# Kernel optimization log

Measured on AMD Instinct MI355X. Metric: run time of the kernel, lower is better.

## Reference

```python
import jax, jax.numpy as jnp
import numpy as np

TINY = 1e-6
SGNUM = 12

def _ln(x, g, b):
    m = jnp.mean(x, -1, keepdims=True)
    v = jnp.mean((x - m) ** 2, -1, keepdims=True)
    return (x - m) * jax.lax.rsqrt(v + 1e-5) * g + b

def _mean_var(x, w):
    # weighted mean/variance over the view dim (-2), keepdim
    mean = jnp.sum(x * w, -2, keepdims=True)
    var = jnp.sum(w * (x - mean) ** 2, -2, keepdims=True)
    return mean, var

def setup_inputs():
    BN, H, W, N = 1, 128, 128, 8
    CTX, PF, PH, HD, MH, FH = 61, 32, 64, 32, 256, 128
    D = CTX + 3 + PF  # 96
    key = jax.random.key(0)
    ks = iter(jax.random.split(key, 64))
    def rnm(shape):
        return jax.random.normal(next(ks), shape, jnp.float32)
    def pw(shape):
        return jax.random.normal(next(ks), shape, jnp.float32) * 0.02
    inp = dict(
        rgb=jax.random.uniform(next(ks), (BN, H, W, N, 3), jnp.float32),
        featmaps_dense=rnm((BN, H, W, 1, CTX)),
        view_dir=rnm((BN, H, W, N, 3)),
        proj_err=rnm((BN, H, W, N, 1)),
        normal=rnm((BN, H, W, 1, 3)),
        DL=rnm((BN, H, W, SGNUM * 7)),
        # pbr_mlp: LN(7) -> Lin(7,PH) ELU -> Lin(PH,PH) ELU -> Lin(PH,PH) ELU -> Lin(PH,PF)
        pbr_ln_g=jnp.ones((7,), jnp.float32), pbr_ln_b=jnp.zeros((7,), jnp.float32),
        pbr_w1=pw((7, PH)), pbr_b1=jnp.zeros((PH,), jnp.float32),
        pbr_w2=pw((PH, PH)), pbr_b2=jnp.zeros((PH,), jnp.float32),
        pbr_w3=pw((PH, PH)), pbr_b3=jnp.zeros((PH,), jnp.float32),
        pbr_w4=pw((PH, PF)), pbr_b4=jnp.zeros((PF,), jnp.float32),
        # transformer block 1
        tv1_ln_g=jnp.ones((D,), jnp.float32), tv1_ln_b=jnp.zeros((D,), jnp.float32),
        tv1_w=pw((D, HD)),
        to1_w=pw((3 * HD, D)), to1_b=jnp.zeros((D,), jnp.float32),
        n1_ln_g=jnp.ones((D,), jnp.float32), n1_ln_b=jnp.zeros((D,), jnp.float32),
        n1_w1=pw((D, MH)), n1_b1=jnp.zeros((MH,), jnp.float32),
        n1_w2=pw((MH, D)), n1_b2=jnp.zeros((D,), jnp.float32),
        # transformer block 2
        tv2_ln_g=jnp.ones((D,), jnp.float32), tv2_ln_b=jnp.zeros((D,), jnp.float32),
        tv2_w=pw((D, HD)),
        to2_w=pw((3 * HD, D)), to2_b=jnp.zeros((D,), jnp.float32),
        n2_ln_g=jnp.ones((D,), jnp.float32), n2_ln_b=jnp.zeros((D,), jnp.float32),
        n2_w1=pw((D, MH)), n2_b1=jnp.zeros((MH,), jnp.float32),
        n2_w2=pw((MH, D)), n2_b2=jnp.zeros((D,), jnp.float32),
        # mlp_brdf
        brdf_ln_g=jnp.ones((D,), jnp.float32), brdf_ln_b=jnp.zeros((D,), jnp.float32),
        brdf_w1=pw((D, FH)), brdf_b1=jnp.zeros((FH,), jnp.float32),
        brdf_w2=pw((FH, FH)), brdf_b2=jnp.zeros((FH,), jnp.float32),
    )
    return inp

def reference(rgb, featmaps_dense, view_dir, proj_err, normal, DL,
              pbr_ln_g, pbr_ln_b, pbr_w1, pbr_b1, pbr_w2, pbr_b2, pbr_w3, pbr_b3, pbr_w4, pbr_b4,
              tv1_ln_g, tv1_ln_b, tv1_w, to1_w, to1_b,
              n1_ln_g, n1_ln_b, n1_w1, n1_b1, n1_w2, n1_b2,
              tv2_ln_g, tv2_ln_b, tv2_w, to2_w, to2_b,
              n2_ln_g, n2_ln_b, n2_w1, n2_b1, n2_w2, n2_b2,
              brdf_ln_g, brdf_ln_b, brdf_w1, brdf_b1, brdf_w2, brdf_b2):
    bn, h, w, n, _ = rgb.shape
    # view weights from reprojection error
    wgt = -jnp.minimum(jnp.log10(jnp.abs(proj_err) + TINY), 0.0)
    wgt = wgt / (jnp.sum(wgt, -2, keepdims=True) + TINY)  # [bn,h,w,n,1]
    DL6 = DL.reshape(bn, h, w, 1, SGNUM, 7)
    dl_dir = DL6[..., :3]
    DLdotN = jnp.sum(dl_dir * normal[:, :, :, :, None, :], -1, keepdims=True)  # [bn,h,w,1,SG,1]
    hdotV = (jnp.sum(dl_dir * view_dir[:, :, :, :, None, :], -1, keepdims=True) + 1.0) * 0.5  # [bn,h,w,n,SG,1]
    fresnel = jnp.exp2((-5.55472 * hdotV - 6.98316) * hdotV)
    VdotN = jnp.sum(view_dir * normal, -1, keepdims=True)[..., None, :]  # [bn,h,w,n,1,1]
    part = jnp.broadcast_to(jnp.concatenate([DLdotN, DL6[..., 3:]], -1), (bn, h, w, n, SGNUM, 5))
    VdotN = jnp.broadcast_to(VdotN, (bn, h, w, n, SGNUM, 1))
    pbr = jnp.concatenate([part, fresnel, VdotN], -1)  # [bn,h,w,n,SG,7]
    y = _ln(pbr, pbr_ln_g, pbr_ln_b)
    y = jax.nn.elu(y @ pbr_w1 + pbr_b1)
    y = jax.nn.elu(y @ pbr_w2 + pbr_b2)
    y = jax.nn.elu(y @ pbr_w3 + pbr_b3)
    pbr_feature = jnp.sum(y @ pbr_w4 + pbr_b4, -2)  # sum over SGNum -> [bn,h,w,n,PF]
    fm = jnp.broadcast_to(featmaps_dense, (bn, h, w, n, featmaps_dense.shape[-1]))
    x_input = jnp.concatenate([rgb, fm, pbr_feature], -1)  # [bn,h,w,n,D]
    # transformer block 1
    v = _ln(x_input, tv1_ln_g, tv1_ln_b) @ tv1_w  # [bn,h,w,n,HD]
    mean, var = _mean_var(v, wgt)
    mv = jnp.broadcast_to(jnp.concatenate([mean, var], -1), v.shape[:-1] + (2 * v.shape[-1],))
    x = jnp.concatenate([v, mv], -1) @ to1_w + to1_b + x_input
    x = jax.nn.gelu(_ln(x, n1_ln_g, n1_ln_b) @ n1_w1 + n1_b1, approximate=False) @ n1_w2 + n1_b2 + x_input
    # transformer block 2 (collapses view dim)
    v = _ln(x, tv2_ln_g, tv2_ln_b) @ tv2_w
    mean, var = _mean_var(v, wgt)
    x = (jnp.concatenate([v[..., :1, :], mean, var], -1) @ to2_w + to2_b)[..., 0, :]
    x = x + x_input[..., 0, :]
    x = jax.nn.gelu(_ln(x, n2_ln_g, n2_ln_b) @ n2_w1 + n2_b1, approximate=False) @ n2_w2 + n2_b2 + x_input[..., 0, :]
    brdf = jax.nn.gelu(_ln(x, brdf_ln_g, brdf_ln_b) @ brdf_w1 + brdf_b1, approximate=False) @ brdf_w2 + brdf_b2
    return brdf  # [bn,h,w,final_hidden]
```

## Files before the change

kernel.cpp:

```cpp
#include <hip/hip_runtime.h>
#include <math.h>


#define NPIX 16384

__device__ __forceinline__ float elu_f(float x){ return x > 0.f ? x : (__expf(x) - 1.f); }
__device__ __forceinline__ float gelu_f(float x){ return 0.5f*x*(1.f + erff(x*0.70710678118654752f)); }

__device__ __forceinline__ void fma4(float4& a, float s, const float4 w){
  a.x = fmaf(s, w.x, a.x); a.y = fmaf(s, w.y, a.y);
  a.z = fmaf(s, w.z, a.z); a.w = fmaf(s, w.w, a.w);
}
__device__ __forceinline__ float4 elu4f(float4 a){
  return make_float4(elu_f(a.x), elu_f(a.y), elu_f(a.z), elu_f(a.w));
}

#define NTA 768
#define NBA (NPIX/2)

constexpr int AYA   = 0;
constexpr int AYB   = 13056;
constexpr int AWB   = 26112;
constexpr int AXL   = 30208;
constexpr int ABIAS = 31744;
constexpr int ATOT  = 31968;

template<int K, int SI, bool DOELU>
__device__ __forceinline__ void mmA64(const float* __restrict__ Xin,
                                      const float* __restrict__ WB,
                                      const float* __restrict__ bias,
                                      float* __restrict__ Yout, int t)
{
  const int rq = t >> 4, c4 = t & 15;
  const float* x0 = Xin + (4*rq+0)*SI;
  const float* x1 = Xin + (4*rq+1)*SI;
  const float* x2 = Xin + (4*rq+2)*SI;
  const float* x3 = Xin + (4*rq+3)*SI;
  const float4* __restrict__ W4 = (const float4*)WB;
  const float4 b = ((const float4*)bias)[c4];
  float4 a0=b, a1=b, a2=b, a3=b;
  #pragma unroll
  for (int k2 = 0; k2 < K/2; ++k2){
    const float2 xa = *(const float2*)(x0 + 2*k2);
    const float2 xb = *(const float2*)(x1 + 2*k2);
    const float2 xc = *(const float2*)(x2 + 2*k2);
    const float2 xd = *(const float2*)(x3 + 2*k2);
    const float4 wA = W4[(2*k2)*16 + c4];
    const float4 wB = W4[(2*k2+1)*16 + c4];
    fma4(a0, xa.x, wA); fma4(a0, xa.y, wB);
    fma4(a1, xb.x, wA); fma4(a1, xb.y, wB);
    fma4(a2, xc.x, wA); fma4(a2, xc.y, wB);
    fma4(a3, xd.x, wA); fma4(a3, xd.y, wB);
  }
  if (DOELU){ a0 = elu4f(a0); a1 = elu4f(a1); a2 = elu4f(a2); a3 = elu4f(a3); }
  *(float4*)(Yout + (4*rq+0)*68 + 4*c4) = a0;
  *(float4*)(Yout + (4*rq+1)*68 + 4*c4) = a1;
  *(float4*)(Yout + (4*rq+2)*68 + 4*c4) = a2;
  *(float4*)(Yout + (4*rq+3)*68 + 4*c4) = a3;
}

__device__ __forceinline__ void mmA32(const float* __restrict__ Xin,
                                      const float* __restrict__ WB,
                                      const float* __restrict__ bias,
                                      float* __restrict__ F, int t)
{
  const int rq = t >> 4, c2 = t & 15;
  const float* x0 = Xin + (4*rq+0)*68;
  const float* x1 = Xin + (4*rq+1)*68;
  const float* x2 = Xin + (4*rq+2)*68;
  const float* x3 = Xin + (4*rq+3)*68;
  const float2* __restrict__ W2 = (const float2*)WB;
  const float2 b = ((const float2*)bias)[c2];
  float2 a0=b, a1=b, a2=b, a3=b;
  #pragma unroll
  for (int k2 = 0; k2 < 32; ++k2){
    const float2 xa = *(const float2*)(x0 + 2*k2);
    const float2 xb = *(const float2*)(x1 + 2*k2);
    const float2 xc = *(const float2*)(x2 + 2*k2);
    const float2 xd = *(const float2*)(x3 + 2*k2);
    const float2 wA = W2[(2*k2)*16 + c2];
    const float2 wB = W2[(2*k2+1)*16 + c2];
    a0.x = fmaf(xa.x, wA.x, a0.x); a0.y = fmaf(xa.x, wA.y, a0.y);
    a0.x = fmaf(xa.y, wB.x, a0.x); a0.y = fmaf(xa.y, wB.y, a0.y);
    a1.x = fmaf(xb.x, wA.x, a1.x); a1.y = fmaf(xb.x, wA.y, a1.y);
    a1.x = fmaf(xb.y, wB.x, a1.x); a1.y = fmaf(xb.y, wB.y, a1.y);
    a2.x = fmaf(xc.x, wA.x, a2.x); a2.y = fmaf(xc.x, wA.y, a2.y);
    a2.x = fmaf(xc.y, wB.x, a2.x); a2.y = fmaf(xc.y, wB.y, a2.y);
    a3.x = fmaf(xd.x, wA.x, a3.x); a3.y = fmaf(xd.x, wA.y, a3.y);
    a3.x = fmaf(xd.y, wB.x, a3.x); a3.y = fmaf(xd.y, wB.y, a3.y);
  }
  *(float2*)(F + (4*rq+0)*34 + 2*c2) = a0;
  *(float2*)(F + (4*rq+1)*34 + 2*c2) = a1;
  *(float2*)(F + (4*rq+2)*34 + 2*c2) = a2;
  *(float2*)(F + (4*rq+3)*34 + 2*c2) = a3;
}

__global__ __launch_bounds__(NTA)
void mva_phaseA(const float* __restrict__ view_dir, const float* __restrict__ normal,
                const float* __restrict__ DL,
                const float* __restrict__ ln_g, const float* __restrict__ ln_b,
                const float* __restrict__ w1, const float* __restrict__ b1,
                const float* __restrict__ w2, const float* __restrict__ b2,
                const float* __restrict__ w3, const float* __restrict__ b3,
                const float* __restrict__ w4, const float* __restrict__ b4,
                float* __restrict__ feat)
{
  __shared__ __align__(16) float smem[ATOT];
  const int t = threadIdx.x;
  const int bpx0 = blockIdx.x*2;
  float4* WB4 = (float4*)(smem + AWB);

  {
    const float4* s = (const float4*)w1;
    for (int i = t; i < 128; i += NTA){
      const int k = i >> 4, c4 = i & 15;
      WB4[i] = (k < 7) ? s[k*16 + c4] : make_float4(0.f,0.f,0.f,0.f);
    }
    float4* d = (float4*)(smem+ABIAS);
    if (t >= 256 && t < 272)      d[t-256]      = ((const float4*)b1)[t-256];
    else if (t >= 272 && t < 288) d[16 + t-272] = ((const float4*)b2)[t-272];
    else if (t >= 288 && t < 304) d[32 + t-288] = ((const float4*)b3)[t-288];
    else if (t >= 304 && t < 312) d[48 + t-304] = ((const float4*)b4)[t-304];
  }
  if (t < 192){
    const int pl = t / 96, rr = t - pl*96;
    const int sg = rr >> 3, view = rr & 7;
    const int px = bpx0 + pl;
    const float nm0 = normal[px*3+0], nm1 = normal[px*3+1], nm2 = normal[px*3+2];
    const float* vd = view_dir + (px*8 + view)*3;
    const float vd0 = vd[0], vd1 = vd[1], vd2 = vd[2];
    const float* dl = DL + px*84 + sg*7;
    const float d0=dl[0], d1=dl[1], d2=dl[2], d3=dl[3], d4=dl[4], d5=dl[5], d6=dl[6];

    const float DLdotN = d0*nm0 + d1*nm1 + d2*nm2;
    const float hv     = (d0*vd0 + d1*vd1 + d2*vd2 + 1.f)*0.5f;
    const float fres   = exp2f((-5.55472f*hv - 6.98316f)*hv);
    const float VdotN  = vd0*nm0 + vd1*nm1 + vd2*nm2;

    const float x0 = DLdotN, x1 = d3, x2 = d4, x3 = d5, x4 = d6, x5 = fres, x6 = VdotN;
    const float m  = (x0+x1+x2+x3+x4+x5+x6)*(1.f/7.f);
    float q, var = 0.f;
    q = x0-m; var += q*q; q = x1-m; var += q*q; q = x2-m; var += q*q;
    q = x3-m; var += q*q; q = x4-m; var += q*q; q = x5-m; var += q*q;
    q = x6-m; var += q*q;
    const float rs = rsqrtf(var*(1.f/7.f) + 1e-5f);
    float* xl = smem + AXL + t*8;
    xl[0] = (x0-m)*rs*ln_g[0] + ln_b[0];
    xl[1] = (x1-m)*rs*ln_g[1] + ln_b[1];
    xl[2] = (x2-m)*rs*ln_g[2] + ln_b[2];
    xl[3] = (x3-m)*rs*ln_g[3] + ln_b[3];
    xl[4] = (x4-m)*rs*ln_g[4] + ln_b[4];
    xl[5] = (x5-m)*rs*ln_g[5] + ln_b[5];
    xl[6] = (x6-m)*rs*ln_g[6] + ln_b[6];
    xl[7] = 0.f;
  }
  __syncthreads();

  float4 p0 = ((const float4*)w2)[t];
  float4 p1 = (t < 256) ? ((const float4*)w2)[t + 768] : make_float4(0.f,0.f,0.f,0.f);
  mmA64<8,8,true>(smem+AXL, smem+AWB, smem+ABIAS+0, smem+AYA, t);
  __syncthreads();
  WB4[t] = p0; if (t < 256) WB4[t + 768] = p1;
  __syncthreads();

  p0 = ((const float4*)w3)[t];
  p1 = (t < 256) ? ((const float4*)w3)[t + 768] : make_float4(0.f,0.f,0.f,0.f);
  mmA64<64,68,true>(smem+AYA, smem+AWB, smem+ABIAS+64, smem+AYB, t);
  __syncthreads();
  WB4[t] = p0; if (t < 256) WB4[t + 768] = p1;
  __syncthreads();

  p0 = (t < 512) ? ((const float4*)w4)[t] : make_float4(0.f,0.f,0.f,0.f);
  mmA64<64,68,true>(smem+AYB, smem+AWB, smem+ABIAS+128, smem+AYA, t);
  __syncthreads();
  if (t < 512) WB4[t] = p0;
  __syncthreads();

  mmA32(smem+AYA, smem+AWB, smem+ABIAS+192, smem+AYB, t);
  __syncthreads();

  if (t < 512){
    const int pl = t >> 8, idx = t & 255;
    const int v = idx >> 5, c = idx & 31;
    float s = 0.f;
    #pragma unroll
    for (int sg = 0; sg < 12; ++sg) s += smem[AYB + (pl*96 + sg*8 + v)*34 + c];
    feat[(size_t)(bpx0 + pl)*256 + idx] = s;
  }
}

#define NTB 512

template<int KK, int CC, int LDWG>
__device__ __forceinline__ void stageW(const float* __restrict__ Wg, int c4off,
                                       float* __restrict__ wbuf, int t)
{
  constexpr int C4 = CC/4;
  constexpr int N4 = KK*C4;
  const float4* __restrict__ s = (const float4*)Wg;
  float4* d = (float4*)wbuf;
  for (int i = t; i < N4; i += NTB){
    const int k = i / C4, c4 = i - k*C4;
    d[i] = s[k*(LDWG/4) + c4off + c4];
  }
}

__device__ __forceinline__ void ln32s(const float* __restrict__ in, int Si,
                                      float* __restrict__ out, int So,
                                      const float* __restrict__ g, const float* __restrict__ b,
                                      int t)
{
  if (t < 256){
    const int r = t >> 3, l8 = t & 7;
    const float* row = in + r*Si;
    float vals[12]; int cols[12];
    float s1 = 0.f, s2 = 0.f;
    #pragma unroll
    for (int i = 0; i < 12; ++i){
      int c = l8 + 8*i + 8*(r & 7); if (c >= 96) c -= 96;
      float a = row[c];
      cols[i] = c; vals[i] = a; s1 += a; s2 += a*a;
    }
    s1 += __shfl_xor(s1, 1); s2 += __shfl_xor(s2, 1);
    s1 += __shfl_xor(s1, 2); s2 += __shfl_xor(s2, 2);
    s1 += __shfl_xor(s1, 4); s2 += __shfl_xor(s2, 4);
    float mean = s1*(1.f/96.f);
    float var  = s2*(1.f/96.f) - mean*mean;
    float rsd = rsqrtf(var + 1e-5f);
    float* orow = out + r*So;
    #pragma unroll
    for (int i = 0; i < 12; ++i){
      int c = cols[i];
      orow[c] = (vals[i]-mean)*rsd*g[c] + b[c];
    }
  }
}

template<int K, int C, int LDW, bool GELU, bool HASB, bool RES, bool ACC>
__device__ __forceinline__ void mmR32(const float* __restrict__ inb, int S,
                                      const float* __restrict__ Wl, const float* __restrict__ bg,
                                      float* __restrict__ outb, int So,
                                      const float* __restrict__ residb, int Sr, int t)
{
  constexpr int C4 = C/4;
  const float4* __restrict__ W4 = (const float4*)Wl;
  for (int gi = t; gi < C4*16; gi += NTB){
    const int rp = gi & 15, c4 = gi >> 4;
    const float2* x0 = (const float2*)(inb + (2*rp)*S);
    const float2* x1 = (const float2*)(inb + (2*rp+1)*S);
    float4 a0 = HASB ? ((const float4*)bg)[c4] : make_float4(0.f,0.f,0.f,0.f);
    float4 a1 = a0;
    #pragma unroll 8
    for (int k2 = 0; k2 < K/2; ++k2){
      float2 xa = x0[k2], xb = x1[k2];
      float4 wA = W4[(2*k2)*(LDW/4) + c4];
      float4 wB = W4[(2*k2+1)*(LDW/4) + c4];
      fma4(a0, xa.x, wA); fma4(a0, xa.y, wB);
      fma4(a1, xb.x, wA); fma4(a1, xb.y, wB);
    }
    if (GELU){
      a0.x=gelu_f(a0.x); a0.y=gelu_f(a0.y); a0.z=gelu_f(a0.z); a0.w=gelu_f(a0.w);
      a1.x=gelu_f(a1.x); a1.y=gelu_f(a1.y); a1.z=gelu_f(a1.z); a1.w=gelu_f(a1.w);
    }
    if (RES){
      const float* r0 = residb + (2*rp)*Sr + 4*c4;
      const float* r1 = residb + (2*rp+1)*Sr + 4*c4;
      a0.x += r0[0]; a0.y += r0[1]; a0.z += r0[2]; a0.w += r0[3];
      a1.x += r1[0]; a1.y += r1[1]; a1.z += r1[2]; a1.w += r1[3];
    }
    float* o0 = outb + (2*rp)*So + 4*c4;
    float* o1 = outb + (2*rp+1)*So + 4*c4;
    if (ACC){
      a0.x += o0[0]; a0.y += o0[1]; a0.z += o0[2]; a0.w += o0[3];
      a1.x += o1[0]; a1.y += o1[1]; a1.z += o1[2]; a1.w += o1[3];
    }
    o0[0]=a0.x; o0[1]=a0.y; o0[2]=a0.z; o0[3]=a0.w;
    o1[0]=a1.x; o1[1]=a1.y; o1[2]=a1.z; o1[3]=a1.w;
  }
}

#define NBB1 (NPIX/4)
constexpr int BXIN  = 0;
constexpr int BXCUR = 3264;
constexpr int BXLN  = 6528;
constexpr int BHID  = 9792;
constexpr int BVB   = 14080;
constexpr int BMEAN = 15296;
constexpr int BVAR  = 15424;
constexpr int BWGT  = 15552;
constexpr int BWBUF = 15584;
constexpr int B1TOT = 27872;

__global__ __launch_bounds__(NTB)
void mva_phaseB1(const float* __restrict__ rgb, const float* __restrict__ fm,
                 const float* __restrict__ proj_err, float* __restrict__ ws,
                 const float* __restrict__ tv1_ln_g, const float* __restrict__ tv1_ln_b,
                 const float* __restrict__ tv1_w,
                 const float* __restrict__ to1_w, const float* __restrict__ to1_b,
                 const float* __restrict__ n1_ln_g, const float* __restrict__ n1_ln_b,
                 const float* __restrict__ n1_w1, const float* __restrict__ n1_b1,
                 const float* __restrict__ n1_w2, const float* __restrict__ n1_b2,
                 const float* __restrict__ tv2_ln_g, const float* __restrict__ tv2_ln_b,
                 const float* __restrict__ tv2_w)
{
  __shared__ __align__(16) float smem[B1TOT];
  const int t = threadIdx.x;
  const int bpx0 = blockIdx.x*4;
  float* WB = smem + BWBUF;

  for (int u = t; u < 2048; u += NTB){
    const int r = u >> 6, k = u & 63;
    const int pl = r >> 3, v = r & 7;
    float val = (k < 3) ? rgb[((bpx0+pl)*8 + v)*3 + k]
                        : fm[(bpx0+pl)*61 + (k-3)];
    smem[BXIN + r*102 + k] = val;
  }
  for (int u = t; u < 1024; u += NTB){
    const int r = u >> 5, c = u & 31;
    smem[BXIN + r*102 + 64 + c] = ws[(size_t)blockIdx.x*1024 + u];
  }
  if (t < 32){
    float pe = proj_err[(bpx0 + (t>>3))*8 + (t&7)];
    float wraw = fmaxf(-log10f(fabsf(pe) + 1e-6f), 0.f);
    float s = wraw;
    s += __shfl_xor(s, 1); s += __shfl_xor(s, 2); s += __shfl_xor(s, 4);
    smem[BWGT + t] = wraw / (s + 1e-6f);
  }
  stageW<96,32,32>(tv1_w, 0, WB, t);
  __syncthreads();

  ln32s(smem+BXIN, 102, smem+BXLN, 102, tv1_ln_g, tv1_ln_b, t);
  __syncthreads();
  mmR32<96,32,32,false,false,false,false>(smem+BXLN, 102, WB, nullptr, smem+BVB, 38, nullptr, 0, t);
  __syncthreads();
  if (t < 128){
    const int pl = t >> 5, c = t & 31;
    const float* wn = smem + BWGT + pl*8;
    float m = 0.f;
    #pragma unroll
    for (int v = 0; v < 8; ++v) m += wn[v]*smem[BVB + (pl*8+v)*38 + c];
    float vv = 0.f;
    #pragma unroll
    for (int v = 0; v < 8; ++v){ float d = smem[BVB + (pl*8+v)*38 + c] - m; vv += wn[v]*d*d; }
    smem[BMEAN + pl*32 + c] = m;
    smem[BVAR  + pl*32 + c] = vv;
  }
  __syncthreads();
  for (int u = t; u < 3072; u += NTB){
    const int r = u & 31, c = u >> 5;
    const int pl = r >> 3;
    float val = (c < 32) ? smem[BVB + r*38 + c]
              : (c < 64) ? smem[BMEAN + pl*32 + (c-32)]
                         : smem[BVAR + pl*32 + (c-64)];
    smem[BXLN + r*102 + c] = val;
  }
  stageW<96,96,96>(to1_w, 0, WB, t);
  __syncthreads();
  mmR32<96,96,96,false,true,true,false>(smem+BXLN, 102, WB, to1_b, smem+BXCUR, 102, smem+BXIN, 102, t);
  __syncthreads();

  ln32s(smem+BXCUR, 102, smem+BXLN, 102, n1_ln_g, n1_ln_b, t);
  __syncthreads();
  stageW<96,128,256>(n1_w1, 0, WB, t);
  __syncthreads();
  mmR32<96,128,128,true,true,false,false>(smem+BXLN, 102, WB, n1_b1, smem+BHID, 134, nullptr, 0, t);
  __syncthreads();
  stageW<128,96,96>(n1_w2, 0, WB, t);
  __syncthreads();
  mmR32<128,96,96,false,false,false,false>(smem+BHID, 134, WB, nullptr, smem+BXCUR, 102, nullptr, 0, t);
  __syncthreads();
  stageW<96,128,256>(n1_w1, 32, WB, t);
  __syncthreads();
  mmR32<96,128,128,true,true,false,false>(smem+BXLN, 102, WB, n1_b1 + 128, smem+BHID, 134, nullptr, 0, t);
  __syncthreads();
  stageW<128,96,96>(n1_w2 + 128*96, 0, WB, t);
  __syncthreads();
  mmR32<128,96,96,false,true,true,true>(smem+BHID, 134, WB, n1_b2, smem+BXCUR, 102, smem+BXIN, 102, t);
  __syncthreads();

  ln32s(smem+BXCUR, 102, smem+BXLN, 102, tv2_ln_g, tv2_ln_b, t);
  stageW<96,32,32>(tv2_w, 0, WB, t);
  __syncthreads();
  mmR32<96,32,32,false,false,false,false>(smem+BXLN, 102, WB, nullptr, smem+BVB, 38, nullptr, 0, t);
  __syncthreads();
  if (t < 128){
    const int pl = t >> 5, c = t & 31;
    const float* wn = smem + BWGT + pl*8;
    float m = 0.f;
    #pragma unroll
    for (int v = 0; v < 8; ++v) m += wn[v]*smem[BVB + (pl*8+v)*38 + c];
    float vv = 0.f;
    #pragma unroll
    for (int v = 0; v < 8; ++v){ float d = smem[BVB + (pl*8+v)*38 + c] - m; vv += wn[v]*d*d; }
    smem[BMEAN + pl*32 + c] = m;
    smem[BVAR  + pl*32 + c] = vv;
  }
  __syncthreads();
  if (t < 384){
    const int pl = t / 96, c = t - pl*96;
    float val = (c < 32) ? smem[BVB + (pl*8)*38 + c]
              : (c < 64) ? smem[BMEAN + pl*32 + (c-32)]
                         : smem[BVAR + pl*32 + (c-64)];
    ws[(size_t)blockIdx.x*1024 + pl*256 + 96 + c] = val;
  }
}

#define NBB2 (NPIX/32)
constexpr int CXLN  = 0;
constexpr int CXIN  = 3264;
constexpr int CXS   = 6528;
constexpr int CTMP  = 9792;
constexpr int CHID  = 13056;
constexpr int CWBUF = 17344;
constexpr int B2TOT = 29632;

__global__ __launch_bounds__(NTB)
void mva_phaseB2(const float* __restrict__ rgb, const float* __restrict__ fm,
                 const float* __restrict__ ws,
                 const float* __restrict__ to2_w, const float* __restrict__ to2_b,
                 const float* __restrict__ n2_ln_g, const float* __restrict__ n2_ln_b,
                 const float* __restrict__ n2_w1, const float* __restrict__ n2_b1,
                 const float* __restrict__ n2_w2, const float* __restrict__ n2_b2,
                 const float* __restrict__ brdf_ln_g, const float* __restrict__ brdf_ln_b,
                 const float* __restrict__ brdf_w1, const float* __restrict__ brdf_b1,
                 const float* __restrict__ brdf_w2, const float* __restrict__ brdf_b2,
                 float* __restrict__ out)
{
  __shared__ __align__(16) float smem[B2TOT];
  const int t = threadIdx.x;
  const int bpx0 = blockIdx.x*32;
  float* WB = smem + CWBUF;

  for (int u = t; u < 3072; u += NTB){
    const int r = u / 96, c = u - r*96;
    const int px = bpx0 + r;
    const size_t ab = (size_t)px*256;
    smem[CXLN + r*102 + c] = ws[ab + 96 + c];
    float xv = (c < 3)  ? rgb[((size_t)px*8)*3 + c]
             : (c < 64) ? fm[(size_t)px*61 + (c-3)]
                        : ws[ab + (c-64)];
    smem[CXIN + r*102 + c] = xv;
  }
  stageW<96,96,96>(to2_w, 0, WB, t);
  __syncthreads();

  mmR32<96,96,96,false,true,true,false>(smem+CXLN, 102, WB, to2_b, smem+CXS, 102, smem+CXIN, 102, t);
  __syncthreads();

  ln32s(smem+CXS, 102, smem+CXLN, 102, n2_ln_g, n2_ln_b, t);
  __syncthreads();
  stageW<96,128,256>(n2_w1, 0, WB, t);
  __syncthreads();
  mmR32<96,128,128,true,true,false,false>(smem+CXLN, 102, WB, n2_b1, smem+CHID, 134, nullptr, 0, t);
  __syncthreads();
  stageW<128,96,96>(n2_w2, 0, WB, t);
  __syncthreads();
  mmR32<128,96,96,false,false,false,false>(smem+CHID, 134, WB, nullptr, smem+CTMP, 102, nullptr, 0, t);
  __syncthreads();
  stageW<96,128,256>(n2_w1, 32, WB, t);
  __syncthreads();
  mmR32<96,128,128,true,true,false,false>(smem+CXLN, 102, WB, n2_b1 + 128, smem+CHID, 134, nullptr, 0, t);
  __syncthreads();
  stageW<128,96,96>(n2_w2 + 128*96, 0, WB, t);
  __syncthreads();
  mmR32<128,96,96,false,true,true,true>(smem+CHID, 134, WB, n2_b2, smem+CTMP, 102, smem+CXIN, 102, t);
  __syncthreads();

  ln32s(smem+CTMP, 102, smem+CXLN, 102, brdf_ln_g, brdf_ln_b, t);
  __syncthreads();
  stageW<96,128,128>(brdf_w1, 0, WB, t);
  __syncthreads();
  mmR32<96,128,128,true,true,false,false>(smem+CXLN, 102, WB, brdf_b1, smem+CHID, 134, nullptr, 0, t);
  __syncthreads();
  float* outp = out + (size_t)bpx0*128;
  stageW<128,64,128>(brdf_w2, 0, WB, t);
  __syncthreads();
  mmR32<128,64,64,false,true,false,false>(smem+CHID, 134, WB, brdf_b2, outp, 128, nullptr, 0, t);
  __syncthreads();
  stageW<128,64,128>(brdf_w2, 16, WB, t);
  __syncthreads();
  mmR32<128,64,64,false,true,false,false>(smem+CHID, 134, WB, brdf_b2 + 64, outp + 64, 128, nullptr, 0, t);
}

extern "C" void kernel_launch(void* const* d_in, const int* in_sizes, int n_in,
                              void* d_out, int out_size, void* d_ws, size_t ws_size,
                              hipStream_t stream)
{
  (void)in_sizes; (void)n_in; (void)ws_size; (void)out_size;
  int i = 0;
  const float* rgb      = (const float*)d_in[i++];
  const float* fm       = (const float*)d_in[i++];
  const float* view_dir = (const float*)d_in[i++];
  const float* proj_err = (const float*)d_in[i++];
  const float* normal   = (const float*)d_in[i++];
  const float* DL       = (const float*)d_in[i++];
  const float* pbr_ln_g = (const float*)d_in[i++];
  const float* pbr_ln_b = (const float*)d_in[i++];
  const float* pbr_w1   = (const float*)d_in[i++];
  const float* pbr_b1   = (const float*)d_in[i++];
  const float* pbr_w2   = (const float*)d_in[i++];
  const float* pbr_b2   = (const float*)d_in[i++];
  const float* pbr_w3   = (const float*)d_in[i++];
  const float* pbr_b3   = (const float*)d_in[i++];
  const float* pbr_w4   = (const float*)d_in[i++];
  const float* pbr_b4   = (const float*)d_in[i++];
  const float* tv1_ln_g = (const float*)d_in[i++];
  const float* tv1_ln_b = (const float*)d_in[i++];
  const float* tv1_w    = (const float*)d_in[i++];
  const float* to1_w    = (const float*)d_in[i++];
  const float* to1_b    = (const float*)d_in[i++];
  const float* n1_ln_g  = (const float*)d_in[i++];
  const float* n1_ln_b  = (const float*)d_in[i++];
  const float* n1_w1    = (const float*)d_in[i++];
  const float* n1_b1    = (const float*)d_in[i++];
  const float* n1_w2    = (const float*)d_in[i++];
  const float* n1_b2    = (const float*)d_in[i++];
  const float* tv2_ln_g = (const float*)d_in[i++];
  const float* tv2_ln_b = (const float*)d_in[i++];
  const float* tv2_w    = (const float*)d_in[i++];
  const float* to2_w    = (const float*)d_in[i++];
  const float* to2_b    = (const float*)d_in[i++];
  const float* n2_ln_g  = (const float*)d_in[i++];
  const float* n2_ln_b  = (const float*)d_in[i++];
  const float* n2_w1    = (const float*)d_in[i++];
  const float* n2_b1    = (const float*)d_in[i++];
  const float* n2_w2    = (const float*)d_in[i++];
  const float* n2_b2    = (const float*)d_in[i++];
  const float* brdf_ln_g= (const float*)d_in[i++];
  const float* brdf_ln_b= (const float*)d_in[i++];
  const float* brdf_w1  = (const float*)d_in[i++];
  const float* brdf_b1  = (const float*)d_in[i++];
  const float* brdf_w2  = (const float*)d_in[i++];
  const float* brdf_b2  = (const float*)d_in[i++];

  float* ws = (float*)d_ws;

  mva_phaseA<<<dim3(NBA), dim3(NTA), 0, stream>>>(
      view_dir, normal, DL, pbr_ln_g, pbr_ln_b,
      pbr_w1, pbr_b1, pbr_w2, pbr_b2, pbr_w3, pbr_b3, pbr_w4, pbr_b4, ws);

  mva_phaseB1<<<dim3(NBB1), dim3(NTB), 0, stream>>>(
      rgb, fm, proj_err, ws,
      tv1_ln_g, tv1_ln_b, tv1_w, to1_w, to1_b,
      n1_ln_g, n1_ln_b, n1_w1, n1_b1, n1_w2, n1_b2,
      tv2_ln_g, tv2_ln_b, tv2_w);

  mva_phaseB2<<<dim3(NBB2), dim3(NTB), 0, stream>>>(
      rgb, fm, ws,
      to2_w, to2_b,
      n2_ln_g, n2_ln_b, n2_w1, n2_b1, n2_w2, n2_b2,
      brdf_ln_g, brdf_ln_b, brdf_w1, brdf_b1, brdf_w2, brdf_b2,
      (float*)d_out);
}
```

Baseline: 1.128 ms.

## Prefetch next weight tile into registers during current matmul

Replaces the synchronous global-to-LDS weight staging between matmul stages with register prefetch. Each thread loads the next stage's weight slice into six float4 registers before the current matmul runs, then writes them to shared memory after it. This hides global load latency behind compute and removes one barrier per stage. It costs 24 extra VGPRs per thread, which may reduce occupancy or cause spills at 512 threads.

```diff
diff --git a/kernel.cpp b/kernel.cpp
--- a/kernel.cpp
+++ b/kernel.cpp
@@ -205,6 +205,22 @@
   }
 }
 
+#define PFSLOT(Wg, KK, CC, LDWG, C4OFF, SLOT, PFV) { \
+  const int _i = t + (SLOT)*512; \
+  if ((KK)*((CC)/4) > (SLOT)*512 && _i < (KK)*((CC)/4)){ \
+    const int _k = _i/((CC)/4), _c = _i - _k*((CC)/4); \
+    PFV = ((const float4*)(Wg))[_k*((LDWG)/4) + (C4OFF) + _c]; } }
+
+#define PFLOADG(Wg, KK, CC, LDWG, C4OFF) \
+  PFSLOT(Wg,KK,CC,LDWG,C4OFF,0,pf0) PFSLOT(Wg,KK,CC,LDWG,C4OFF,1,pf1) \
+  PFSLOT(Wg,KK,CC,LDWG,C4OFF,2,pf2) PFSLOT(Wg,KK,CC,LDWG,C4OFF,3,pf3) \
+  PFSLOT(Wg,KK,CC,LDWG,C4OFF,4,pf4) PFSLOT(Wg,KK,CC,LDWG,C4OFF,5,pf5)
+
+#define PFWR(N4, SLOT, PFV) { if ((N4) > (SLOT)*512 && t + (SLOT)*512 < (N4)) WB4[t+(SLOT)*512] = PFV; }
+#define PFWRITE(KK, CC) { \
+  PFWR((KK)*((CC)/4),0,pf0) PFWR((KK)*((CC)/4),1,pf1) PFWR((KK)*((CC)/4),2,pf2) \
+  PFWR((KK)*((CC)/4),3,pf3) PFWR((KK)*((CC)/4),4,pf4) PFWR((KK)*((CC)/4),5,pf5) }
+
 __device__ __forceinline__ void ln32s(const float* __restrict__ in, int Si,
                                       float* __restrict__ out, int So,
                                       const float* __restrict__ g, const float* __restrict__ b,
@@ -307,6 +323,8 @@
   const int t = threadIdx.x;
   const int bpx0 = blockIdx.x*4;
   float* WB = smem + BWBUF;
+  float4* WB4 = (float4*)WB;
+  float4 pf0 = make_float4(0,0,0,0), pf1 = pf0, pf2 = pf0, pf3 = pf0, pf4 = pf0, pf5 = pf0;
 
   for (int u = t; u < 2048; u += NTB){
     const int r = u >> 6, k = u & 63;
@@ -330,6 +348,7 @@
   __syncthreads();
 
   ln32s(smem+BXIN, 102, smem+BXLN, 102, tv1_ln_g, tv1_ln_b, t);
+  PFLOADG(to1_w, 96,96,96, 0)
   __syncthreads();
   mmR32<96,32,32,false,false,false,false>(smem+BXLN, 102, WB, nullptr, smem+BVB, 38, nullptr, 0, t);
   __syncthreads();
@@ -345,6 +364,7 @@
     smem[BMEAN + pl*32 + c] = m;
     smem[BVAR  + pl*32 + c] = vv;
   }
+  PFWRITE(96,96)
   __syncthreads();
   for (int u = t; u < 3072; u += NTB){
     const int r = u & 31, c = u >> 5;
@@ -354,32 +374,33 @@
                          : smem[BVAR + pl*32 + (c-64)];
     smem[BXLN + r*102 + c] = val;
   }
-  stageW<96,96,96>(to1_w, 0, WB, t);
-  __syncthreads();
+  __syncthreads();
+  PFLOADG(n1_w1, 96,128,256, 0)
   mmR32<96,96,96,false,true,true,false>(smem+BXLN, 102, WB, to1_b, smem+BXCUR, 102, smem+BXIN, 102, t);
   __syncthreads();
-
   ln32s(smem+BXCUR, 102, smem+BXLN, 102, n1_ln_g, n1_ln_b, t);
-  __syncthreads();
-  stageW<96,128,256>(n1_w1, 0, WB, t);
-  __syncthreads();
+  PFWRITE(96,128)
+  __syncthreads();
+  PFLOADG(n1_w2, 128,96,96, 0)
   mmR32<96,128,128,true,true,false,false>(smem+BXLN, 102, WB, n1_b1, smem+BHID, 134, nullptr, 0, t);
   __syncthreads();
-  stageW<128,96,96>(n1_w2, 0, WB, t);
-  __syncthreads();
+  PFWRITE(128,96)
+  __syncthreads();
+  PFLOADG(n1_w1, 96,128,256, 32)
   mmR32<128,96,96,false,false,false,false>(smem+BHID, 134, WB, nullptr, smem+BXCUR, 102, nullptr, 0, t);
   __syncthreads();
-  stageW<96,128,256>(n1_w1, 32, WB, t);
-  __syncthreads();
+  PFWRITE(96,128)
+  __syncthreads();
+  PFLOADG(n1_w2 + 128*96, 128,96,96, 0)
   mmR32<96,128,128,true,true,false,false>(smem+BXLN, 102, WB, n1_b1 + 128, smem+BHID, 134, nullptr, 0, t);
   __syncthreads();
-  stageW<128,96,96>(n1_w2 + 128*96, 0, WB, t);
-  __syncthreads();
+  PFWRITE(128,96)
+  __syncthreads();
+  PFLOADG(tv2_w, 96,32,32, 0)
   mmR32<128,96,96,false,true,true,true>(smem+BHID, 134, WB, n1_b2, smem+BXCUR, 102, smem+BXIN, 102, t);
   __syncthreads();
-
   ln32s(smem+BXCUR, 102, smem+BXLN, 102, tv2_ln_g, tv2_ln_b, t);
-  stageW<96,32,32>(tv2_w, 0, WB, t);
+  PFWRITE(96,32)
   __syncthreads();
   mmR32<96,32,32,false,false,false,false>(smem+BXLN, 102, WB, nullptr, smem+BVB, 38, nullptr, 0, t);
   __syncthreads();
@@ -430,6 +451,8 @@
   const int t = threadIdx.x;
   const int bpx0 = blockIdx.x*32;
   float* WB = smem + CWBUF;
+  float4* WB4 = (float4*)WB;
+  float4 pf0 = make_float4(0,0,0,0), pf1 = pf0, pf2 = pf0, pf3 = pf0, pf4 = pf0, pf5 = pf0;
 
   for (int u = t; u < 3072; u += NTB){
     const int r = u / 96, c = u - r*96;
@@ -444,40 +467,43 @@
   stageW<96,96,96>(to2_w, 0, WB, t);
   __syncthreads();
 
+  PFLOADG(n2_w1, 96,128,256, 0)
   mmR32<96,96,96,false,true,true,false>(smem+CXLN, 102, WB, to2_b, smem+CXS, 102, smem+CXIN, 102, t);
   __syncthreads();
-
   ln32s(smem+CXS, 102, smem+CXLN, 102, n2_ln_g, n2_ln_b, t);
-  __syncthreads();
-  stageW<96,128,256>(n2_w1, 0, WB, t);
-  __syncthreads();
+  PFWRITE(96,128)
+  __syncthreads();
+  PFLOADG(n2_w2, 128,96,96, 0)
   mmR32<96,128,128,true,true,false,false>(smem+CXLN, 102, WB, n2_b1, smem+CHID, 134, nullptr, 0, t);
   __syncthreads();
-  stageW<128,96,96>(n2_w2, 0, WB, t);
-  __syncthreads();
+  PFWRITE(128,96)
+  __syncthreads();
+  PFLOADG(n2_w1, 96,128,256, 32)
   mmR32<128,96,96,false,false,false,false>(smem+CHID, 134, WB, nullptr, smem+CTMP, 102, nullptr, 0, t);
   __syncthreads();
-  stageW<96,128,256>(n2_w1, 32, WB, t);
-  __syncthreads();
+  PFWRITE(96,128)
+  __syncthreads();
+  PFLOADG(n2_w2 + 128*96, 128,96,96, 0)
   mmR32<96,128,128,true,true,false,false>(smem+CXLN, 102, WB, n2_b1 + 128, smem+CHID, 134, nullptr, 0, t);
   __syncthreads();
-  stageW<128,96,96>(n2_w2 + 128*96, 0, WB, t);
-  __syncthreads();
+  PFWRITE(128,96)
+  __syncthreads();
+  PFLOADG(brdf_w1, 96,128,128, 0)
   mmR32<128,96,96,false,true,true,true>(smem+CHID, 134, WB, n2_b2, smem+CTMP, 102, smem+CXIN, 102, t);
   __syncthreads();
-
   ln32s(smem+CTMP, 102, smem+CXLN, 102, brdf_ln_g, brdf_ln_b, t);
-  __syncthreads();
-  stageW<96,128,128>(brdf_w1, 0, WB, t);
-  __syncthreads();
+  PFWRITE(96,128)
+  __syncthreads();
+  PFLOADG(brdf_w2, 128,64,128, 0)
   mmR32<96,128,128,true,true,false,false>(smem+CXLN, 102, WB, brdf_b1, smem+CHID, 134, nullptr, 0, t);
   __syncthreads();
+  PFWRITE(128,64)
+  __syncthreads();
   float* outp = out + (size_t)bpx0*128;
-  stageW<128,64,128>(brdf_w2, 0, WB, t);
-  __syncthreads();
+  PFLOADG(brdf_w2, 128,64,128, 16)
   mmR32<128,64,64,false,true,false,false>(smem+CHID, 134, WB, brdf_b2, outp, 128, nullptr, 0, t);
   __syncthreads();
-  stageW<128,64,128>(brdf_w2, 16, WB, t);
+  PFWRITE(128,64)
   __syncthreads();
   mmR32<128,64,64,false,true,false,false>(smem+CHID, 134, WB, brdf_b2 + 64, outp + 64, 128, nullptr, 0, t);
 }
```

New measurement: 1.087 ms, median of 2. -3.6%, faster.
